# Optimization experiments

Hardware: AMD Instinct MI355X
Metric: run time of the kernel (lower is better)

The kernel has to match this reference:

```python
import jax, jax.numpy as jnp
import numpy as np

THRESHOLD = 0.5
SLACK = 3
EPS = 1e-12
B, H, W = 16, 512, 512


def _shift(p, dy, dx, b, h, w):
    # p is zero-padded by 1 on spatial dims; returns neighbor at offset (dy, dx)
    return p[:, 1 + dy:1 + dy + h, 1 + dx:1 + dx + w]


def _thin_sub(img, step):
    # One Zhang-Suen sub-iteration on bool image [B,H,W] (zero boundary, as skimage)
    b, h, w = img.shape
    p = jnp.pad(img.astype(jnp.int32), ((0, 0), (1, 1), (1, 1)))
    # P2..P9 clockwise starting at North
    P2 = _shift(p, -1, 0, b, h, w); P3 = _shift(p, -1, 1, b, h, w)
    P4 = _shift(p, 0, 1, b, h, w);  P5 = _shift(p, 1, 1, b, h, w)
    P6 = _shift(p, 1, 0, b, h, w);  P7 = _shift(p, 1, -1, b, h, w)
    P8 = _shift(p, 0, -1, b, h, w); P9 = _shift(p, -1, -1, b, h, w)
    seq = [P2, P3, P4, P5, P6, P7, P8, P9, P2]
    Bn = P2 + P3 + P4 + P5 + P6 + P7 + P8 + P9          # neighbor count
    A = sum((1 - seq[k]) * seq[k + 1] for k in range(8))  # 0->1 transitions
    cond = (Bn >= 2) & (Bn <= 6) & (A == 1)
    if step == 0:
        cond = cond & (P2 * P4 * P6 == 0) & (P4 * P6 * P8 == 0)
    else:
        cond = cond & (P2 * P4 * P8 == 0) & (P2 * P6 * P8 == 0)
    return img & ~cond


def _skeletonize(img):
    # Iterate Zhang-Suen thinning to convergence (skimage.morphology.skeletonize 2D = Zhang's method)
    def body(state):
        cur, _ = state
        nxt = _thin_sub(_thin_sub(cur, 0), 1)
        return (nxt, jnp.any(nxt != cur))

    out, _ = jax.lax.while_loop(lambda s: s[1], body, (img, jnp.array(True)))
    return out


def _edt_sq(mask):
    # Exact squared Euclidean distance to nearest True pixel, separable 2-pass.
    b, h, w = mask.shape
    BIG = h + w  # larger than any attainable 1D distance
    g = jnp.where(mask, 0, BIG).astype(jnp.int32)  # [B,H,W]

    # pass 1: 1D nearest-True distance along rows (axis=1) via fwd/bwd scans
    def fscan(carry, row):
        d = jnp.minimum(row, carry + 1)
        return d, d

    g_rows = jnp.moveaxis(g, 1, 0)  # [H,B,W]
    init = jnp.full((b, w), BIG, jnp.int32)
    _, fwd = jax.lax.scan(fscan, init, g_rows)
    _, bwd = jax.lax.scan(fscan, init, g_rows[::-1])
    f = jnp.minimum(jnp.minimum(fwd, bwd[::-1]), BIG)  # [H,B,W]
    f2 = jnp.moveaxis(f * f, 0, 1)  # [B,H,W] squared vertical distance

    # pass 2: d2[b,i,j] = min_{j'} f2[b,i,j'] + (j-j')^2 (lower envelope, memory-friendly lax.map)
    js = jnp.arange(w, dtype=jnp.int32)

    def one_col(j):
        off = (js - j) ** 2  # [W]
        return jnp.min(f2 + off[None, None, :], axis=-1)  # [B,H]

    d2 = jax.lax.map(one_col, js)  # [W,B,H]
    return jnp.transpose(d2, (1, 2, 0))  # [B,H,W]


def setup_inputs() -> dict:
    key = jax.random.key(0)
    k1, k2 = jax.random.split(key)
    y_pred = jax.random.uniform(k1, (B, H, W), dtype=jnp.float32)
    y_true = jax.random.uniform(k2, (B, H, W), dtype=jnp.float32)
    return {"y_pred": y_pred, "y_true": y_true}


def reference(y_pred, y_true):
    p = y_pred > THRESHOLD  # greater_is_road=True binarization
    g = y_true > THRESHOLD
    p = _skeletonize(p)
    g = _skeletonize(g)
    d2_gt = _edt_sq(g)   # EDT of ~g == distance to nearest g pixel
    d2_pr = _edt_sq(p)
    s2 = SLACK * SLACK   # dist <= slack  <=>  dist^2 <= slack^2 (integer sq EDT)
    tp_area = d2_gt <= s2
    fp_area = ~tp_area
    fn_area = d2_pr > s2
    ax = (1, 2)
    TP = jnp.sum(tp_area & p, ax).astype(jnp.float32)
    FP = jnp.sum(fp_area & p, ax).astype(jnp.float32)
    FN = jnp.sum(fn_area & g, ax).astype(jnp.float32)
    correctness = TP / (TP + FP + EPS)
    completeness = TP / (TP + FN + EPS)
    quality = TP / (TP + FP + FN + EPS)
    # mean over batch -> [3]: [correctness, completeness, quality]
    return jnp.mean(jnp.stack([correctness, completeness, quality], axis=1), axis=0)
```

## Files before the change

kernel.cpp:

```cpp
#include <hip/hip_runtime.h>
#include <stdint.h>

#define HH 512
#define WW 512
#define HW (HH * WW)
#define WPR 8
#define NWORDS (HH * WPR)
#define NTHREADS 1024
#define NB 16
#define NIMG (2 * NB)

#define LSTR 10
#define LROWS (HH + 2)
#define LWORDS (LROWS * LSTR)

typedef unsigned long long u64;

__device__ __forceinline__ u64 zs_core(u64 cc, u64 P2, u64 P3, u64 P4, u64 P5,
                                       u64 P6, u64 P7, u64 P8, u64 P9, int step) {
    u64 ab = P2 ^ P3;
    u64 s1 = ab ^ P4, c1 = (P2 & P3) | (ab & P4);
    u64 de = P5 ^ P6;
    u64 s2 = de ^ P7, c2 = (P5 & P6) | (de & P7);
    u64 s3 = P8 ^ P9, c3 = P8 & P9;
    u64 gh = s1 ^ s2;
    u64 b0 = gh ^ s3, c4 = (s1 & s2) | (gh & s3);
    u64 ij = c1 ^ c2;
    u64 s4 = ij ^ c3, c5 = (c1 & c2) | (ij & c3);
    u64 b1 = s4 ^ c4, c6 = s4 & c4;
    u64 b2 = c5 ^ c6, b3 = c5 & c6;

    u64 Bge2 = b1 | b2 | b3;
    u64 Ble6 = ~(b3 | (b2 & b1 & b0));

    u64 a1, a2, t;
    t = ~P2 & P3; a1 = t; a2 = 0ULL;
    t = ~P3 & P4; a2 |= a1 & t; a1 |= t;
    t = ~P4 & P5; a2 |= a1 & t; a1 |= t;
    t = ~P5 & P6; a2 |= a1 & t; a1 |= t;
    t = ~P6 & P7; a2 |= a1 & t; a1 |= t;
    t = ~P7 & P8; a2 |= a1 & t; a1 |= t;
    t = ~P8 & P9; a2 |= a1 & t; a1 |= t;
    t = ~P9 & P2; a2 |= a1 & t; a1 |= t;
    u64 Aeq1 = a1 & ~a2;

    u64 sccond = (step == 0) ? ~((P4 & P6) & (P2 | P8))
                             : ~((P2 & P8) & (P4 | P6));

    return cc & ~(Bge2 & Ble6 & Aeq1 & sccond);
}

__device__ __forceinline__ u64 spread4(u64 x) {
    x = (x | (x << 24)) & 0x000000FF000000FFULL;
    x = (x | (x << 12)) & 0x000F000F000F000FULL;
    x = (x | (x << 6))  & 0x0303030303030303ULL;
    x = (x | (x << 3))  & 0x1111111111111111ULL;
    return x;
}

__global__ __launch_bounds__(256)
void pack_kernel(const float* __restrict__ y_pred,
                 const float* __restrict__ y_true,
                 u64* __restrict__ bits ,
                 int* __restrict__ cnt ) {
    int tid = threadIdx.x;
    if (blockIdx.x == 0 && tid < 4 * NB + NIMG + 1) cnt[tid] = 0;

    int t = blockIdx.x * 256 + tid;
    int lane = tid & 63;
    size_t p0 = (size_t)t * 4;
    const float* src;
    size_t off;
    if (p0 < (size_t)NB * HW) { src = y_pred; off = p0; }
    else                      { src = y_true; off = p0 - (size_t)NB * HW; }
    float4 a = *(const float4*)(src + off);
    unsigned nib = (unsigned)(a.x > 0.5f)
                 | ((unsigned)(a.y > 0.5f) << 1)
                 | ((unsigned)(a.z > 0.5f) << 2)
                 | ((unsigned)(a.w > 0.5f) << 3);
    u64 b0 = __ballot(nib & 1u);
    u64 b1 = __ballot(nib & 2u);
    u64 b2 = __ballot(nib & 4u);
    u64 b3 = __ballot(nib & 8u);
    if (lane < 4) {
        unsigned sh = lane * 16;
        u64 w = spread4((b0 >> sh) & 0xFFFFu)
              | (spread4((b1 >> sh) & 0xFFFFu) << 1)
              | (spread4((b2 >> sh) & 0xFFFFu) << 2)
              | (spread4((b3 >> sh) & 0xFFFFu) << 3);
        size_t wave = (size_t)t >> 6;
        bits[wave * 4 + lane] = w;
    }
}

#define SSTRIPS 8
#define SIROWS (HH / SSTRIPS)
#define SHALO 24
#define SDROWS (SIROWS + 2 * SHALO)
#define STHREADS (SDROWS * WPR)
#define SITERS (SHALO / 2)
#define SSTR 10
#define SLWORDS ((SDROWS + 2) * SSTR)

__global__ __launch_bounds__(STHREADS)
void strip_kernel(const u64* __restrict__ src, u64* __restrict__ dst,
                  int* __restrict__ flags, int rec) {
    __shared__ u64 Mb[2][SLWORDS];
    __shared__ unsigned int Cpb[2][SDROWS + 2];
    __shared__ int s_any[3];

    int bx = blockIdx.x;
    int img = bx >> 3;
    int s = bx & 7;
    int tid = threadIdx.x;
    int lane = tid & 63;
    int r = tid >> 3;
    int c = tid & 7;
    int gr = s * SIROWS - SHALO + r;

    for (int i = tid; i < SLWORDS; i += STHREADS) { Mb[0][i] = 0; Mb[1][i] = 0; }
    if (tid < SDROWS + 2) {
        Cpb[0][tid] = (tid >= 1 && tid <= SDROWS) ? 0x1FEu : 0u;
        Cpb[1][tid] = 0u;
    }
    if (tid < 3) s_any[tid] = 0;
    __syncthreads();

    const u64* gsrc = src + (size_t)img * NWORDS;
    u64 v = (gr >= 0 && gr < HH) ? gsrc[gr * WPR + c] : 0ULL;
    int base = (r + 1) * SSTR + (c + 1);
    Mb[0][base] = v;

    unsigned dl = 0x1FEu;
    bool prevchg = true;
    int it = 0;
    bool done = false;
    for (;;) {
        for (int step = 0; step < 2; ++step) {
            __syncthreads();
            if (step == 0 && it > 0) {
                if (s_any[(it + 2) % 3] == 0) { done = true; break; }
            }
            const u64* Ms = Mb[step];
            u64* Md = Mb[step ^ 1];
            const unsigned* CpS = Cpb[step];
            unsigned* CpD = Cpb[step ^ 1];

            unsigned need = ((CpS[r] | CpS[r + 1] | CpS[r + 2]) >> c) & 7u;
            bool chg = false;
            if (need) {
                u64 cc = Ms[base];
                u64 nv = cc;
                if (cc) {
                    u64 nm = Ms[base - SSTR - 1], nc = Ms[base - SSTR], np = Ms[base - SSTR + 1];
                    u64 cm = Ms[base - 1],                              cp = Ms[base + 1];
                    u64 sm = Ms[base + SSTR - 1], sc = Ms[base + SSTR], sp = Ms[base + SSTR + 1];
                    u64 P2 = nc;
                    u64 P3 = (nc >> 1) | (np << 63);
                    u64 P4 = (cc >> 1) | (cp << 63);
                    u64 P5 = (sc >> 1) | (sp << 63);
                    u64 P6 = sc;
                    u64 P7 = (sc << 1) | (sm >> 63);
                    u64 P8 = (cc << 1) | (cm >> 63);
                    u64 P9 = (nc << 1) | (nm >> 63);
                    nv = zs_core(cc, P2, P3, P4, P5, P6, P7, P8, P9, step);
                    chg = (nv != cc);
                }
                if (chg | prevchg) Md[base] = nv;
            }
            prevchg = chg;
            u64 bal = __ballot(chg);
            if (bal && lane == 0) s_any[it % 3] = 1;
            if ((lane & 7) == 0) {
                unsigned byte = ((unsigned)(bal >> lane) & 0xFFu) << 1;
                CpD[r + 1] = byte | dl;
                dl = byte;
            }
            if (step == 1 && tid == 0) s_any[(it + 1) % 3] = 0;
        }
        if (done) break;
        if (++it >= SITERS) break;
    }
    __syncthreads();
    int lastAny = done ? 0 : s_any[(SITERS - 1) % 3];

    if (r >= SHALO && r < SHALO + SIROWS) {
        dst[(size_t)img * NWORDS + gr * WPR + c] = Mb[0][base];
    }
    if (rec && lastAny && tid == 0) flags[img] = 1;
}

__global__ __launch_bounds__(NTHREADS, 4)
void skel_kernel(u64* __restrict__ bits, const int* __restrict__ flags) {
    __shared__ u64 Mb[2][LWORDS];
    __shared__ unsigned int Cpb[2][130];
    __shared__ int s_any[3];

    int bx = blockIdx.x;
    if (flags[bx] == 0) return;

    int tid = threadIdx.x;
    int lane = tid & 63;
    int c = tid & 7;
    int rb = tid >> 3;

    u64* gm = bits + (size_t)bx * NWORDS;

    if (tid < LROWS) {
        int i = tid;
        if (i == 0 || i == LROWS - 1) {
            #pragma unroll
            for (int j = 0; j < LSTR; ++j) { Mb[0][i * LSTR + j] = 0; Mb[1][i * LSTR + j] = 0; }
        } else {
            Mb[0][i * LSTR + 0] = 0; Mb[0][i * LSTR + 9] = 0;
            Mb[1][i * LSTR + 0] = 0; Mb[1][i * LSTR + 9] = 0;
        }
    }
    {
        const ulonglong2* s2 = (const ulonglong2*)gm;
        #pragma unroll
        for (int k = 0; k < 2; ++k) {
            int i = k * NTHREADS + tid;
            ulonglong2 v = s2[i];
            int wi = i * 2;
            int r = wi >> 3, c2 = wi & 7;
            int li = (r + 1) * LSTR + c2 + 1;
            Mb[0][li] = v.x;
            Mb[0][li + 1] = v.y;
        }
    }
    if (tid < 130) {
        Cpb[0][tid] = (tid >= 1 && tid <= 128) ? 0x1FEu : 0u;
        Cpb[1][tid] = 0u;
    }
    if (tid < 3) s_any[tid] = 0;

    unsigned dl = 0x1FEu;
    bool prevchg = true;
    int base = (rb * 4 + 1) * LSTR + (c + 1);

    int it = 0;
    bool done = false;
    for (;;) {
        for (int step = 0; step < 2; ++step) {
            __syncthreads();
            if (step == 0 && it > 0) {
                if (s_any[(it + 2) % 3] == 0) { done = true; break; }
            }
            const u64* Ms = Mb[step];
            u64* Md = Mb[step ^ 1];
            const unsigned* CpS = Cpb[step];
            unsigned* CpD = Cpb[step ^ 1];

            unsigned need = ((CpS[rb] | CpS[rb + 1] | CpS[rb + 2]) >> c) & 7u;
            bool chg = false;
            if (need) {
                u64 Ca, Ea, Wa, Cb, Eb, Wb, Cc, Ec, Wc;
                {   int a = base - LSTR;
                    u64 x = Ms[a], mm = Ms[a - 1], pp = Ms[a + 1];
                    Ca = x; Ea = (x >> 1) | (pp << 63); Wa = (x << 1) | (mm >> 63); }
                {   int a = base;
                    u64 x = Ms[a], mm = Ms[a - 1], pp = Ms[a + 1];
                    Cb = x; Eb = (x >> 1) | (pp << 63); Wb = (x << 1) | (mm >> 63); }
                u64 nv0 = 0, nv1 = 0, nv2 = 0, nv3 = 0;
                {   int a = base + LSTR;
                    u64 x = Ms[a], mm = Ms[a - 1], pp = Ms[a + 1];
                    Cc = x; Ec = (x >> 1) | (pp << 63); Wc = (x << 1) | (mm >> 63);
                    if (Cb) nv0 = zs_core(Cb, Ca, Ea, Eb, Ec, Cc, Wc, Wb, Wa, step);
                    chg |= (nv0 != Cb);
                    Ca = Cb; Ea = Eb; Wa = Wb; Cb = Cc; Eb = Ec; Wb = Wc; }
                {   int a = base + 2 * LSTR;
                    u64 x = Ms[a], mm = Ms[a - 1], pp = Ms[a + 1];
                    Cc = x; Ec = (x >> 1) | (pp << 63); Wc = (x << 1) | (mm >> 63);
                    if (Cb) nv1 = zs_core(Cb, Ca, Ea, Eb, Ec, Cc, Wc, Wb, Wa, step);
                    chg |= (nv1 != Cb);
                    Ca = Cb; Ea = Eb; Wa = Wb; Cb = Cc; Eb = Ec; Wb = Wc; }
                {   int a = base + 3 * LSTR;
                    u64 x = Ms[a], mm = Ms[a - 1], pp = Ms[a + 1];
                    Cc = x; Ec = (x >> 1) | (pp << 63); Wc = (x << 1) | (mm >> 63);
                    if (Cb) nv2 = zs_core(Cb, Ca, Ea, Eb, Ec, Cc, Wc, Wb, Wa, step);
                    chg |= (nv2 != Cb);
                    Ca = Cb; Ea = Eb; Wa = Wb; Cb = Cc; Eb = Ec; Wb = Wc; }
                {   int a = base + 4 * LSTR;
                    u64 x = Ms[a], mm = Ms[a - 1], pp = Ms[a + 1];
                    Cc = x; Ec = (x >> 1) | (pp << 63); Wc = (x << 1) | (mm >> 63);
                    if (Cb) nv3 = zs_core(Cb, Ca, Ea, Eb, Ec, Cc, Wc, Wb, Wa, step);
                    chg |= (nv3 != Cb); }
                if (chg | prevchg) {
                    Md[base] = nv0;
                    Md[base + LSTR] = nv1;
                    Md[base + 2 * LSTR] = nv2;
                    Md[base + 3 * LSTR] = nv3;
                }
            }
            prevchg = chg;
            u64 bal = __ballot(chg);
            if (bal && lane == 0) s_any[it % 3] = 1;
            if ((lane & 7) == 0) {
                unsigned byte = ((unsigned)(bal >> lane) & 0xFFu) << 1;
                CpD[rb + 1] = byte | dl;
                dl = byte;
            }
            if (step == 1 && tid == 0) s_any[(it + 1) % 3] = 0;
        }
        if (done || it >= 1024) break;
        ++it;
    }

    {
        ulonglong2* d2 = (ulonglong2*)gm;
        #pragma unroll
        for (int k = 0; k < 2; ++k) {
            int i = k * NTHREADS + tid;
            int wi = i * 2;
            int r = wi >> 3, c2 = wi & 7;
            int li = (r + 1) * LSTR + c2 + 1;
            ulonglong2 v;
            v.x = Mb[0][li];
            v.y = Mb[0][li + 1];
            d2[i] = v;
        }
    }
}

#define STRIPS 8
#define SROWS (HH / STRIPS)
#define SR2 (SROWS + 6)

__device__ __forceinline__ u64 ldws(const u64* M, int r, int c) {
    return (c < 0 || c >= WPR) ? 0ULL : M[r * WPR + c];
}

__device__ __forceinline__ u64 dil3s(const u64* M, int r, int c) {
    u64 cm = ldws(M, r, c - 1), cc = ldws(M, r, c), cp = ldws(M, r, c + 1);
    u64 h = cc
          | (cc >> 1) | (cp << 63)
          | (cc >> 2) | (cp << 62)
          | (cc >> 3) | (cp << 61)
          | (cc << 1) | (cm >> 63)
          | (cc << 2) | (cm >> 62)
          | (cc << 3) | (cm >> 61);
    u64 um = ldws(M, r - 1, c - 1) | ldws(M, r + 1, c - 1) | ldws(M, r - 2, c - 1) | ldws(M, r + 2, c - 1);
    u64 uc = ldws(M, r - 1, c    ) | ldws(M, r + 1, c    ) | ldws(M, r - 2, c    ) | ldws(M, r + 2, c    );
    u64 up = ldws(M, r - 1, c + 1) | ldws(M, r + 1, c + 1) | ldws(M, r - 2, c + 1) | ldws(M, r + 2, c + 1);
    h |= uc
       | (uc >> 1) | (up << 63)
       | (uc >> 2) | (up << 62)
       | (uc << 1) | (um >> 63)
       | (uc << 2) | (um >> 62);
    h |= ldws(M, r - 3, c) | ldws(M, r + 3, c);
    return h;
}

__global__ __launch_bounds__(256)
void count_kernel(const u64* __restrict__ skel, int* __restrict__ cnt,
                  int* __restrict__ done, float* __restrict__ out) {
    __shared__ u64 P[SR2 * WPR];
    __shared__ u64 G[SR2 * WPR];
    __shared__ int acc[4];
    __shared__ int s_last;

    int b = blockIdx.x / STRIPS;
    int s = blockIdx.x % STRIPS;
    int tid = threadIdx.x;
    int r0 = s * SROWS - 3;

    const u64* sp = skel + (size_t)b * NWORDS;
    const u64* sg = skel + (size_t)(NB + b) * NWORDS;
    for (int i = tid; i < SR2 * WPR; i += 256) {
        int gr = r0 + (i >> 3);
        bool in = (gr >= 0 && gr < HH);
        int gi = gr * WPR + (i & 7);
        P[i] = in ? sp[gi] : 0ULL;
        G[i] = in ? sg[gi] : 0ULL;
    }
    if (tid < 4) acc[tid] = 0;
    __syncthreads();

    int cp = 0, cg = 0, tp = 0, fnh = 0;
    #pragma unroll
    for (int k = 0; k < 2; ++k) {
        int w = k * 256 + tid;
        int r = (w >> 3) + 3, c = w & 7;
        u64 pw = P[r * WPR + c], gw = G[r * WPR + c];
        cp  += __popcll(pw);
        cg  += __popcll(gw);
        tp  += __popcll(pw & dil3s(G, r, c));
        fnh += __popcll(gw & dil3s(P, r, c));
    }
    #pragma unroll
    for (int o = 32; o > 0; o >>= 1) {
        cp  += __shfl_down(cp, o);
        cg  += __shfl_down(cg, o);
        tp  += __shfl_down(tp, o);
        fnh += __shfl_down(fnh, o);
    }
    if ((tid & 63) == 0) {
        atomicAdd(&acc[0], cp);
        atomicAdd(&acc[1], cg);
        atomicAdd(&acc[2], tp);
        atomicAdd(&acc[3], fnh);
    }
    __syncthreads();
    if (tid < 4) atomicAdd(&cnt[b * 4 + tid], acc[tid]);
    __syncthreads();
    if (tid == 0) {
        __threadfence();
        s_last = (atomicAdd(done, 1) == NB * STRIPS - 1);
    }
    __syncthreads();
    if (!s_last) return;
    __threadfence();

    if (tid < 3) {
        float sacc = 0.0f;
        for (int i = 0; i < NB; ++i) {
            float c0 = (float)atomicAdd(&cnt[i * 4 + 0], 0);
            float c1 = (float)atomicAdd(&cnt[i * 4 + 1], 0);
            float TP = (float)atomicAdd(&cnt[i * 4 + 2], 0);
            float c3 = (float)atomicAdd(&cnt[i * 4 + 3], 0);
            float FP = c0 - TP;
            float FN = c1 - c3;
            float v = (tid == 0) ? TP / (TP + FP + 1e-12f)
                    : (tid == 1) ? TP / (TP + FN + 1e-12f)
                                 : TP / (TP + FP + FN + 1e-12f);
            sacc += v;
        }
        out[tid] = sacc * (1.0f / NB);
    }
}

extern "C" void kernel_launch(void* const* d_in, const int* in_sizes, int n_in,
                              void* d_out, int out_size, void* d_ws, size_t ws_size,
                              hipStream_t stream) {
    (void)in_sizes; (void)n_in; (void)out_size; (void)ws_size;
    const float* y_pred = (const float*)d_in[0];
    const float* y_true = (const float*)d_in[1];
    float* out = (float*)d_out;

    u64* buf1 = (u64*)d_ws;
    u64* buf2 = buf1 + (size_t)NIMG * NWORDS;
    int* cnt = (int*)(buf2 + (size_t)NIMG * NWORDS);
    int* flags = cnt + 4 * NB;
    int* done = flags + NIMG;

    hipLaunchKernelGGL(pack_kernel, dim3(2 * NB * HW / 4 / 256), dim3(256), 0, stream,
                       y_pred, y_true, buf1, cnt);
    hipLaunchKernelGGL(strip_kernel, dim3(NIMG * SSTRIPS), dim3(STHREADS), 0, stream,
                       buf1, buf2, flags, 0);
    hipLaunchKernelGGL(strip_kernel, dim3(NIMG * SSTRIPS), dim3(STHREADS), 0, stream,
                       buf2, buf1, flags, 1);
    hipLaunchKernelGGL(skel_kernel, dim3(NIMG), dim3(NTHREADS), 0, stream,
                       buf1, flags);
    hipLaunchKernelGGL(count_kernel, dim3(NB * STRIPS), dim3(256), 0, stream,
                       buf1, cnt, done, out);
}
```

Baseline: 112.6 us.

## Fuse strip thinning passes and counting into one cooperative kernel with grid sync

Replaces the two fixed strip passes, the whole-image skel kernel and the count kernel with a single cooperative kernel. It repeats halo-strip thinning passes across the grid, separated by grid.sync, until no image changes, then does the slack-dilation counting in the same launch. This removes launch overhead and the slow single-block-per-image convergence phase. In exchange it adds a grid-wide barrier per pass and requires all 256 blocks to be co-resident, falling back to the old path if the cooperative launch fails.

```diff
diff --git a/kernel.cpp b/kernel.cpp
--- a/kernel.cpp
+++ b/kernel.cpp
@@ -1,18 +1,16 @@
 #include <hip/hip_runtime.h>
+#include <hip/hip_cooperative_groups.h>
 #include <stdint.h>
+
+namespace cg = cooperative_groups;
 
 #define HH 512
 #define WW 512
 #define HW (HH * WW)
 #define WPR 8
 #define NWORDS (HH * WPR)
-#define NTHREADS 1024
 #define NB 16
 #define NIMG (2 * NB)
-
-#define LSTR 10
-#define LROWS (HH + 2)
-#define LWORDS (LROWS * LSTR)
 
 typedef unsigned long long u64;
 
@@ -62,9 +60,9 @@
 void pack_kernel(const float* __restrict__ y_pred,
                  const float* __restrict__ y_true,
                  u64* __restrict__ bits ,
-                 int* __restrict__ cnt ) {
+                 int* __restrict__ cnt) {
     int tid = threadIdx.x;
-    if (blockIdx.x == 0 && tid < 4 * NB + NIMG + 1) cnt[tid] = 0;
+    if (blockIdx.x == 0 && tid < 4 * NB + 3 * NIMG + 1) cnt[tid] = 0;
 
     int t = blockIdx.x * 256 + tid;
     int lane = tid & 63;
@@ -97,17 +95,51 @@
 #define SIROWS (HH / SSTRIPS)
 #define SHALO 24
 #define SDROWS (SIROWS + 2 * SHALO)
-#define STHREADS (SDROWS * WPR)
+#define CTHREADS (SDROWS * WPR)
 #define SITERS (SHALO / 2)
 #define SSTR 10
 #define SLWORDS ((SDROWS + 2) * SSTR)
-
-__global__ __launch_bounds__(STHREADS)
-void strip_kernel(const u64* __restrict__ src, u64* __restrict__ dst,
-                  int* __restrict__ flags, int rec) {
+#define MAXPASS 24
+
+#define STRIPS 8
+#define SROWS (HH / STRIPS)
+#define SR2 (SROWS + 6)
+
+__device__ __forceinline__ u64 ldws(const u64* M, int r, int c) {
+    return (c < 0 || c >= WPR) ? 0ULL : M[r * WPR + c];
+}
+
+__device__ __forceinline__ u64 dil3s(const u64* M, int r, int c) {
+    u64 cm = ldws(M, r, c - 1), cc = ldws(M, r, c), cp = ldws(M, r, c + 1);
+    u64 h = cc
+          | (cc >> 1) | (cp << 63)
+          | (cc >> 2) | (cp << 62)
+          | (cc >> 3) | (cp << 61)
+          | (cc << 1) | (cm >> 63)
+          | (cc << 2) | (cm >> 62)
+          | (cc << 3) | (cm >> 61);
+    u64 um = ldws(M, r - 1, c - 1) | ldws(M, r + 1, c - 1) | ldws(M, r - 2, c - 1) | ldws(M, r + 2, c - 1);
+    u64 uc = ldws(M, r - 1, c    ) | ldws(M, r + 1, c    ) | ldws(M, r - 2, c    ) | ldws(M, r + 2, c    );
+    u64 up = ldws(M, r - 1, c + 1) | ldws(M, r + 1, c + 1) | ldws(M, r - 2, c + 1) | ldws(M, r + 2, c + 1);
+    h |= uc
+       | (uc >> 1) | (up << 63)
+       | (uc >> 2) | (up << 62)
+       | (uc << 1) | (um >> 63)
+       | (uc << 2) | (um >> 62);
+    h |= ldws(M, r - 3, c) | ldws(M, r + 3, c);
+    return h;
+}
+
+__global__ __launch_bounds__(CTHREADS, 4)
+void coop_kernel(u64* __restrict__ buf0, u64* __restrict__ buf1,
+                 int* __restrict__ cnt, int* __restrict__ flags ,
+                 int* __restrict__ done, float* __restrict__ out) {
+    cg::grid_group grid = cg::this_grid();
     __shared__ u64 Mb[2][SLWORDS];
     __shared__ unsigned int Cpb[2][SDROWS + 2];
     __shared__ int s_any[3];
+    __shared__ int s_acc[4];
+    __shared__ int s_lastf;
 
     int bx = blockIdx.x;
     int img = bx >> 3;
@@ -117,8 +149,179 @@
     int r = tid >> 3;
     int c = tid & 7;
     int gr = s * SIROWS - SHALO + r;
-
-    for (int i = tid; i < SLWORDS; i += STHREADS) { Mb[0][i] = 0; Mb[1][i] = 0; }
+    bool grin = (gr >= 0 && gr < HH);
+    int gw = gr * WPR + c;
+    int base = (r + 1) * SSTR + (c + 1);
+
+    int fin = 0;
+    for (int p = 0; p < MAXPASS; ++p) {
+        const u64* src = ((p & 1) ? buf1 : buf0) + (size_t)img * NWORDS;
+        u64* dst = ((p & 1) ? buf0 : buf1) + (size_t)img * NWORDS;
+        if (s == 0 && tid == 0) flags[((p + 1) % 3) * NIMG + img] = 0;
+
+        for (int i = tid; i < SLWORDS; i += CTHREADS) { Mb[0][i] = 0; Mb[1][i] = 0; }
+        if (tid < SDROWS + 2) {
+            Cpb[0][tid] = (tid >= 1 && tid <= SDROWS) ? 0x1FEu : 0u;
+            Cpb[1][tid] = 0u;
+        }
+        if (tid < 3) s_any[tid] = 0;
+        __syncthreads();
+        Mb[0][base] = grin ? src[gw] : 0ULL;
+
+        unsigned dl = 0x1FEu;
+        bool prevchg = true;
+        int it = 0;
+        bool ldone = false;
+        for (;;) {
+            for (int step = 0; step < 2; ++step) {
+                __syncthreads();
+                if (step == 0 && it > 0) {
+                    if (s_any[(it + 2) % 3] == 0) { ldone = true; break; }
+                }
+                const u64* Ms = Mb[step];
+                u64* Md = Mb[step ^ 1];
+                const unsigned* CpS = Cpb[step];
+                unsigned* CpD = Cpb[step ^ 1];
+
+                unsigned need = ((CpS[r] | CpS[r + 1] | CpS[r + 2]) >> c) & 7u;
+                bool chg = false;
+                if (need) {
+                    u64 cc = Ms[base];
+                    u64 nv = cc;
+                    if (cc) {
+                        u64 nm = Ms[base - SSTR - 1], nc = Ms[base - SSTR], np = Ms[base - SSTR + 1];
+                        u64 cm = Ms[base - 1],                              cp = Ms[base + 1];
+                        u64 sm = Ms[base + SSTR - 1], sc = Ms[base + SSTR], sp = Ms[base + SSTR + 1];
+                        u64 P2 = nc;
+                        u64 P3 = (nc >> 1) | (np << 63);
+                        u64 P4 = (cc >> 1) | (cp << 63);
+                        u64 P5 = (sc >> 1) | (sp << 63);
+                        u64 P6 = sc;
+                        u64 P7 = (sc << 1) | (sm >> 63);
+                        u64 P8 = (cc << 1) | (cm >> 63);
+                        u64 P9 = (nc << 1) | (nm >> 63);
+                        nv = zs_core(cc, P2, P3, P4, P5, P6, P7, P8, P9, step);
+                        chg = (nv != cc);
+                    }
+                    if (chg | prevchg) Md[base] = nv;
+                }
+                prevchg = chg;
+                u64 bal = __ballot(chg);
+                if (bal && lane == 0) s_any[it % 3] = 1;
+                if ((lane & 7) == 0) {
+                    unsigned byte = ((unsigned)(bal >> lane) & 0xFFu) << 1;
+                    CpD[r + 1] = byte | dl;
+                    dl = byte;
+                }
+                if (step == 1 && tid == 0) s_any[(it + 1) % 3] = 0;
+            }
+            if (ldone) break;
+            if (++it >= SITERS) break;
+        }
+        __syncthreads();
+        int lastAny = ldone ? 0 : s_any[(SITERS - 1) % 3];
+
+        if (r >= SHALO && r < SHALO + SIROWS) dst[gw] = Mb[0][base];
+        if (lastAny && tid == 0) flags[(p % 3) * NIMG + img] = 1;
+
+        grid.sync();
+
+        int any = 0;
+        const int* f = flags + (p % 3) * NIMG;
+        for (int i = 0; i < NIMG; ++i) any |= f[i];
+        fin = (p + 1) & 1;
+        if (!any) break;
+    }
+
+    if (bx >= NB * STRIPS) return;
+    {
+        u64* Pl = Mb[0];
+        u64* Gl = Mb[1];
+        int b = bx >> 3;
+        int cs = bx & 7;
+        int r0 = cs * SROWS - 3;
+        const u64* fb = fin ? buf1 : buf0;
+        const u64* sp = fb + (size_t)b * NWORDS;
+        const u64* sg = fb + (size_t)(NB + b) * NWORDS;
+        for (int i = tid; i < SR2 * WPR; i += CTHREADS) {
+            int grr = r0 + (i >> 3);
+            bool in = (grr >= 0 && grr < HH);
+            int gi = grr * WPR + (i & 7);
+            Pl[i] = in ? sp[gi] : 0ULL;
+            Gl[i] = in ? sg[gi] : 0ULL;
+        }
+        if (tid < 4) s_acc[tid] = 0;
+        __syncthreads();
+
+        int cp = 0, cg2 = 0, tp = 0, fnh = 0;
+        if (tid < SROWS * WPR) {
+            int rr = (tid >> 3) + 3, c2 = tid & 7;
+            u64 pw = Pl[rr * WPR + c2], gw2 = Gl[rr * WPR + c2];
+            cp  = __popcll(pw);
+            cg2 = __popcll(gw2);
+            tp  = __popcll(pw & dil3s(Gl, rr, c2));
+            fnh = __popcll(gw2 & dil3s(Pl, rr, c2));
+        }
+        #pragma unroll
+        for (int o = 32; o > 0; o >>= 1) {
+            cp  += __shfl_down(cp, o);
+            cg2 += __shfl_down(cg2, o);
+            tp  += __shfl_down(tp, o);
+            fnh += __shfl_down(fnh, o);
+        }
+        if (lane == 0) {
+            atomicAdd(&s_acc[0], cp);
+            atomicAdd(&s_acc[1], cg2);
+            atomicAdd(&s_acc[2], tp);
+            atomicAdd(&s_acc[3], fnh);
+        }
+        __syncthreads();
+        if (tid < 4) atomicAdd(&cnt[b * 4 + tid], s_acc[tid]);
+        __syncthreads();
+        if (tid == 0) {
+            __threadfence();
+            s_lastf = (atomicAdd(done, 1) == NB * STRIPS - 1);
+        }
+        __syncthreads();
+        if (!s_lastf) return;
+        __threadfence();
+
+        if (tid < 3) {
+            float sacc = 0.0f;
+            for (int i = 0; i < NB; ++i) {
+                float c0 = (float)atomicAdd(&cnt[i * 4 + 0], 0);
+                float c1 = (float)atomicAdd(&cnt[i * 4 + 1], 0);
+                float TP = (float)atomicAdd(&cnt[i * 4 + 2], 0);
+                float c3 = (float)atomicAdd(&cnt[i * 4 + 3], 0);
+                float FP = c0 - TP;
+                float FN = c1 - c3;
+                float v = (tid == 0) ? TP / (TP + FP + 1e-12f)
+                        : (tid == 1) ? TP / (TP + FN + 1e-12f)
+                                     : TP / (TP + FP + FN + 1e-12f);
+                sacc += v;
+            }
+            out[tid] = sacc * (1.0f / NB);
+        }
+    }
+}
+
+__global__ __launch_bounds__(CTHREADS)
+void strip_kernel(const u64* __restrict__ src, u64* __restrict__ dst,
+                  int* __restrict__ flags, int rec) {
+    __shared__ u64 Mb[2][SLWORDS];
+    __shared__ unsigned int Cpb[2][SDROWS + 2];
+    __shared__ int s_any[3];
+
+    int bx = blockIdx.x;
+    int img = bx >> 3;
+    int s = bx & 7;
+    int tid = threadIdx.x;
+    int lane = tid & 63;
+    int r = tid >> 3;
+    int c = tid & 7;
+    int gr = s * SIROWS - SHALO + r;
+
+    for (int i = tid; i < SLWORDS; i += CTHREADS) { Mb[0][i] = 0; Mb[1][i] = 0; }
     if (tid < SDROWS + 2) {
         Cpb[0][tid] = (tid >= 1 && tid <= SDROWS) ? 0x1FEu : 0u;
         Cpb[1][tid] = 0u;
@@ -145,7 +348,6 @@
             u64* Md = Mb[step ^ 1];
             const unsigned* CpS = Cpb[step];
             unsigned* CpD = Cpb[step ^ 1];
-
             unsigned need = ((CpS[r] | CpS[r + 1] | CpS[r + 2]) >> c) & 7u;
             bool chg = false;
             if (need) {
@@ -183,12 +385,16 @@
     }
     __syncthreads();
     int lastAny = done ? 0 : s_any[(SITERS - 1) % 3];
-
     if (r >= SHALO && r < SHALO + SIROWS) {
         dst[(size_t)img * NWORDS + gr * WPR + c] = Mb[0][base];
     }
     if (rec && lastAny && tid == 0) flags[img] = 1;
 }
+
+#define LSTR 10
+#define LROWS (HH + 2)
+#define LWORDS (LROWS * LSTR)
+#define NTHREADS 1024
 
 __global__ __launch_bounds__(NTHREADS, 4)
 void skel_kernel(u64* __restrict__ bits, const int* __restrict__ flags) {
@@ -251,7 +457,6 @@
             u64* Md = Mb[step ^ 1];
             const unsigned* CpS = Cpb[step];
             unsigned* CpD = Cpb[step ^ 1];
-
             unsigned need = ((CpS[rb] | CpS[rb + 1] | CpS[rb + 2]) >> c) & 7u;
             bool chg = false;
             if (need) {
@@ -323,35 +528,6 @@
     }
 }
 
-#define STRIPS 8
-#define SROWS (HH / STRIPS)
-#define SR2 (SROWS + 6)
-
-__device__ __forceinline__ u64 ldws(const u64* M, int r, int c) {
-    return (c < 0 || c >= WPR) ? 0ULL : M[r * WPR + c];
-}
-
-__device__ __forceinline__ u64 dil3s(const u64* M, int r, int c) {
-    u64 cm = ldws(M, r, c - 1), cc = ldws(M, r, c), cp = ldws(M, r, c + 1);
-    u64 h = cc
-          | (cc >> 1) | (cp << 63)
-          | (cc >> 2) | (cp << 62)
-          | (cc >> 3) | (cp << 61)
-          | (cc << 1) | (cm >> 63)
-          | (cc << 2) | (cm >> 62)
-          | (cc << 3) | (cm >> 61);
-    u64 um = ldws(M, r - 1, c - 1) | ldws(M, r + 1, c - 1) | ldws(M, r - 2, c - 1) | ldws(M, r + 2, c - 1);
-    u64 uc = ldws(M, r - 1, c    ) | ldws(M, r + 1, c    ) | ldws(M, r - 2, c    ) | ldws(M, r + 2, c    );
-    u64 up = ldws(M, r - 1, c + 1) | ldws(M, r + 1, c + 1) | ldws(M, r - 2, c + 1) | ldws(M, r + 2, c + 1);
-    h |= uc
-       | (uc >> 1) | (up << 63)
-       | (uc >> 2) | (up << 62)
-       | (uc << 1) | (um >> 63)
-       | (uc << 2) | (um >> 62);
-    h |= ldws(M, r - 3, c) | ldws(M, r + 3, c);
-    return h;
-}
-
 __global__ __launch_bounds__(256)
 void count_kernel(const u64* __restrict__ skel, int* __restrict__ cnt,
                   int* __restrict__ done, float* __restrict__ out) {
@@ -438,20 +614,32 @@
     const float* y_true = (const float*)d_in[1];
     float* out = (float*)d_out;
 
-    u64* buf1 = (u64*)d_ws;
-    u64* buf2 = buf1 + (size_t)NIMG * NWORDS;
-    int* cnt = (int*)(buf2 + (size_t)NIMG * NWORDS);
+    u64* buf0 = (u64*)d_ws;
+    u64* buf1 = buf0 + (size_t)NIMG * NWORDS;
+    int* cnt = (int*)(buf1 + (size_t)NIMG * NWORDS);
     int* flags = cnt + 4 * NB;
-    int* done = flags + NIMG;
+    int* done = flags + 3 * NIMG;
 
     hipLaunchKernelGGL(pack_kernel, dim3(2 * NB * HW / 4 / 256), dim3(256), 0, stream,
-                       y_pred, y_true, buf1, cnt);
-    hipLaunchKernelGGL(strip_kernel, dim3(NIMG * SSTRIPS), dim3(STHREADS), 0, stream,
-                       buf1, buf2, flags, 0);
-    hipLaunchKernelGGL(strip_kernel, dim3(NIMG * SSTRIPS), dim3(STHREADS), 0, stream,
-                       buf2, buf1, flags, 1);
-    hipLaunchKernelGGL(skel_kernel, dim3(NIMG), dim3(NTHREADS), 0, stream,
-                       buf1, flags);
-    hipLaunchKernelGGL(count_kernel, dim3(NB * STRIPS), dim3(256), 0, stream,
-                       buf1, cnt, done, out);
-}
+                       y_pred, y_true, buf0, cnt);
+
+    {
+        u64* a0 = buf0; u64* a1 = buf1;
+        int* ac = cnt; int* af = flags; int* ad = done;
+        float* ao = out;
+        void* args[] = {&a0, &a1, &ac, &af, &ad, &ao};
+        hipError_t e = hipLaunchCooperativeKernel((const void*)coop_kernel,
+                                                  dim3(NIMG * SSTRIPS), dim3(CTHREADS),
+                                                  args, 0, stream);
+        if (e != hipSuccess) {
+            hipLaunchKernelGGL(strip_kernel, dim3(NIMG * SSTRIPS), dim3(CTHREADS), 0, stream,
+                               buf0, buf1, flags, 0);
+            hipLaunchKernelGGL(strip_kernel, dim3(NIMG * SSTRIPS), dim3(CTHREADS), 0, stream,
+                               buf1, buf0, flags, 1);
+            hipLaunchKernelGGL(skel_kernel, dim3(NIMG), dim3(NTHREADS), 0, stream,
+                               buf0, flags);
+            hipLaunchKernelGGL(count_kernel, dim3(NB * STRIPS), dim3(256), 0, stream,
+                               buf0, cnt, done, out);
+        }
+    }
+}
```

After: 147.5 us. 1.31x slower.
